# Performance work log

Measured on AMD Instinct MI355X. Metric: run time of the kernel, lower is better.

## Reference

```python
import jax, jax.numpy as jnp
import numpy as np

EMBED = 50
SEQ = 100
NLABEL = 15
HID = 20
VOCAB = 50000
BATCH = 8192


def gru_scan(xs, W, U, b, return_sequences):
    """Keras GRUCell (reset_after=True, gate order z,r,h).
    xs: (B, T, D). W: (D, 3H), U: (H, 3H), b: (2, 3H) [input bias, recurrent bias].
    """
    B = xs.shape[0]
    H = U.shape[0]
    bi, br = b[0], b[1]
    h0 = jnp.zeros((B, H), dtype=xs.dtype)

    def step(h, x_t):
        mx = x_t @ W + bi                      # (B, 3H)
        mh = h @ U + br                        # (B, 3H)
        xz, xr, xh = mx[:, :H], mx[:, H:2*H], mx[:, 2*H:]
        hz, hr, hh_ = mh[:, :H], mh[:, H:2*H], mh[:, 2*H:]
        z = jax.nn.sigmoid(xz + hz)
        r = jax.nn.sigmoid(xr + hr)
        hh = jnp.tanh(xh + r * hh_)
        h_new = z * h + (1.0 - z) * hh
        return h_new, h_new

    xs_t = jnp.swapaxes(xs, 0, 1)              # (T, B, D)
    h_last, hs = jax.lax.scan(step, h0, xs_t)
    if return_sequences:
        return jnp.swapaxes(hs, 0, 1)          # (B, T, H)
    return h_last                               # (B, H)


def setup_inputs() -> dict:
    key = jax.random.key(0)
    ks = jax.random.split(key, 9)
    s = 0.05
    return {
        "x": jax.random.randint(ks[0], (BATCH, SEQ), 0, VOCAB),
        "emb_table": jax.random.normal(ks[1], (VOCAB, EMBED), jnp.float32) * s,
        "W1": jax.random.normal(ks[2], (EMBED, 3 * HID), jnp.float32) * s,
        "U1": jax.random.normal(ks[3], (HID, 3 * HID), jnp.float32) * s,
        "b1": jnp.zeros((2, 3 * HID), jnp.float32),
        "W2": jax.random.normal(ks[4], (HID, 3 * HID), jnp.float32) * s,
        "U2": jax.random.normal(ks[5], (HID, 3 * HID), jnp.float32) * s,
        "b2": jnp.zeros((2, 3 * HID), jnp.float32),
        "Wd": jax.random.normal(ks[6], (HID, NLABEL), jnp.float32) * s,
        "bd": jnp.zeros((NLABEL,), jnp.float32),
        "drop_rate": 0,
    }


def reference(x, emb_table, W1, U1, b1, W2, U2, b2, Wd, bd, drop_rate):
    emb = emb_table[x]                               # (B, T, E)
    seq = gru_scan(emb, W1, U1, b1, return_sequences=True)   # (B, T, H)
    enc = gru_scan(seq, W2, U2, b2, return_sequences=False)  # (B, H)
    # drop_rate == 0 -> tf.nn.dropout is identity
    logits = enc @ Wd + bd                           # (B, 15)
    return logits
```

## Files before the change

### kernel.cpp

```cpp
#include <hip/hip_runtime.h>
#include <hip/hip_bf16.h>
#include <hip/hip_fp16.h>

#define SEQ_T 100
#define HID 20
#define EMB_D 50
#define VOCAB_N 50000
#define TABW 60
#define NTILE 3125
#define BBLK 782

typedef short sh8 __attribute__((ext_vector_type(8)));
typedef float f4  __attribute__((ext_vector_type(4)));

#define OFF_U1P 0
#define OFF_W2P 600
#define OFF_U2P 1200
#define OFF_B1  3600
#define OFF_B2  3720
#define OFF_WD  3840
#define OFF_BD  4140
#define OFF_TAB 4160

__device__ __forceinline__ float ldf(const void* p, int i, int isf) {
  return isf ? ((const float*)p)[i]
             : __bfloat162float(((const __hip_bfloat16*)p)[i]);
}
__device__ __forceinline__ short f2bf(float f) {
  unsigned u = __float_as_uint(f);
  u += 0x7fffu + ((u >> 16) & 1u);
  return (short)(u >> 16);
}
__device__ __forceinline__ float rdl(float v, int l) {
  return __uint_as_float(__builtin_amdgcn_readlane(__float_as_uint(v), l));
}
__device__ __forceinline__ int detect_isf(const void* emb) {
  uint4 dv = ((const uint4*)emb)[threadIdx.x & 63];
  int big = 0;
#pragma unroll
  for (int i = 0; i < 4; ++i) {
    unsigned w = ((const unsigned*)&dv)[i];
    big |= (((w >> 7) & 0xFF) >= 140) | (((w >> 23) & 0xFF) >= 140);
  }
  return (__ballot(big) != 0ull) ? 1 : 0;
}

__global__ __launch_bounds__(256) void build_table(
    const void* __restrict__ emb, const void* __restrict__ W1,
    const void* __restrict__ b1,
    const void* __restrict__ U1, const void* __restrict__ W2,
    const void* __restrict__ U2, const void* __restrict__ b2,
    const void* __restrict__ Wd, const void* __restrict__ bd,
    float* __restrict__ ws)
{
  const int isf = detect_isf(emb);
  if (blockIdx.x == 0) {
    const int t = threadIdx.x;
    unsigned* wsu = (unsigned*)ws;
    for (int i = t; i < 600; i += 256) {
      const int j = i / 10, p = i % 10;
      const int k0 = 2 * p, k1 = 2 * p + 1;
#define PK(M) ((unsigned)__half_as_ushort(__float2half_rn(ldf(M, k0 * 60 + j, isf))) | \
               ((unsigned)__half_as_ushort(__float2half_rn(ldf(M, k1 * 60 + j, isf))) << 16))
      wsu[OFF_U1P + i] = PK(U1);
      wsu[OFF_W2P + i] = PK(W2);
      wsu[OFF_U2P + i] = PK(U2);
#undef PK
    }
    for (int i = t; i < 120; i += 256) {
      ws[OFF_B1 + i] = ldf(b1, i, isf);
      ws[OFF_B2 + i] = ldf(b2, i, isf);
    }
    for (int i = t; i < 300; i += 256) ws[OFF_WD + i] = ldf(Wd, i, isf);
    for (int i = t; i < 15;  i += 256) ws[OFF_BD + i] = ldf(bd, i, isf);
  }

  const int L = threadIdx.x & 63, q = L >> 4, c = L & 15;
  const int wid = blockIdx.x * 4 + (threadIdx.x >> 6);
  float* __restrict__ tab = ws + OFF_TAB;

  __shared__ int4 sB[64][8];
  if (threadIdx.x < 64) {
#pragma unroll
    for (int nt = 0; nt < 4; ++nt) {
      const int col = nt * 16 + c;
      sh8 B0, B1;
#pragma unroll
      for (int jj = 0; jj < 8; ++jj) {
        const int k0 = q * 8 + jj, k1 = 32 + q * 8 + jj;
        B0[jj] = (col < TABW) ? f2bf(ldf(W1, k0 * TABW + col, isf)) : (short)0;
        B1[jj] = (col < TABW && k1 < EMB_D)
                     ? f2bf(ldf(W1, k1 * TABW + col, isf)) : (short)0;
      }
      sB[L][nt * 2]     = *(const int4*)&B0;
      sB[L][nt * 2 + 1] = *(const int4*)&B1;
    }
  }
  float bi[4];
#pragma unroll
  for (int nt = 0; nt < 4; ++nt) {
    const int col = nt * 16 + c;
    bi[nt] = (col < TABW) ? ldf(b1, col, isf) : 0.f;
  }
  __syncthreads();

  for (int tile = wid; tile < NTILE; tile += BBLK * 4) {
    const int v0 = tile * 16;
    sh8 A0, A1;
#pragma unroll
    for (int jj = 0; jj < 8; ++jj) { A0[jj] = 0; A1[jj] = 0; }
    if (!isf) {
      const unsigned short* eb = (const unsigned short*)emb;
      const size_t rb = (size_t)(v0 + c) * EMB_D;
#pragma unroll
      for (int i = 0; i < 4; ++i) {
        unsigned d = *(const unsigned*)(eb + rb + q * 8 + 2 * i);
        A0[2 * i] = (short)(d & 0xffff); A0[2 * i + 1] = (short)(d >> 16);
      }
      const int k1b = 32 + q * 8;
#pragma unroll
      for (int i = 0; i < 4; ++i) {
        const int k = k1b + 2 * i;
        if (k + 1 < EMB_D) {
          unsigned d = *(const unsigned*)(eb + rb + k);
          A1[2 * i] = (short)(d & 0xffff); A1[2 * i + 1] = (short)(d >> 16);
        }
      }
    } else {
      const float* ef = (const float*)emb;
      const size_t rb = (size_t)(v0 + c) * EMB_D;
#pragma unroll
      for (int jj = 0; jj < 8; ++jj) {
        const int k0 = q * 8 + jj, k1 = 32 + q * 8 + jj;
        A0[jj] = f2bf(ef[rb + k0]);
        A1[jj] = (k1 < EMB_D) ? f2bf(ef[rb + k1]) : (short)0;
      }
    }
#pragma unroll
    for (int nt = 0; nt < 4; ++nt) {
      int4 b0i = sB[L][nt * 2], b1i = sB[L][nt * 2 + 1];
      sh8 B0 = *(const sh8*)&b0i, B1 = *(const sh8*)&b1i;
      const int col = nt * 16 + c;
      f4 acc = { bi[nt], bi[nt], bi[nt], bi[nt] };
      acc = __builtin_amdgcn_mfma_f32_16x16x32_bf16(A0, B0, acc, 0, 0, 0);
      acc = __builtin_amdgcn_mfma_f32_16x16x32_bf16(A1, B1, acc, 0, 0, 0);
      if (col < TABW) {
#pragma unroll
        for (int r = 0; r < 4; ++r)
          tab[(size_t)(v0 + q * 4 + r) * TABW + col] = acc[r];
      }
    }
  }
}

__global__ __launch_bounds__(256, 6) void gru_main(
    const int* __restrict__ x, const float* __restrict__ ws,
    const void* __restrict__ emb, void* __restrict__ out)
{
  const int isf = detect_isf(emb);
  const int j = threadIdx.x & 63;
  const int e = __builtin_amdgcn_readfirstlane(blockIdx.x * 4 + (threadIdx.x >> 6));
  const int jc = j < TABW ? j : 0;

  const int* xr = x + (size_t)e * SEQ_T;
  const float* tab = ws + OFF_TAB;
  const int o1 = jc * 40;
  const int jc4 = jc * 4;
  const int a1 = ((j - 20) & 63) * 4;
  const int a2 = ((j + 40) & 63) * 4;
  const float br1 = ws[OFF_B1 + 60 + jc];
  const float bi2 = ws[OFF_B2 + jc];
  const float br2 = ws[OFF_B2 + 60 + jc];

  __shared__ char sbuf[1024];
  const unsigned lb = (unsigned)(uintptr_t)&sbuf[0] + (threadIdx.x >> 6) * 256;
  const int wad = (int)(lb + (j < 20 ? 2 * j : 40 + 2 * (j - 20)));
  const int rad = (int)lb;
  float h2out;

  asm volatile(
    "global_load_dwordx4 v[10:13], %[o1], %[wsp] offset:0\n\t"
    "global_load_dwordx4 v[14:17], %[o1], %[wsp] offset:16\n\t"
    "global_load_dwordx2 v[18:19], %[o1], %[wsp] offset:32\n\t"
    "v_add_u32 v44, 0x960, %[o1]\n\t"
    "v_add_u32 v45, 0x12c0, %[o1]\n\t"
    "global_load_dwordx4 v[20:23], v44, %[wsp] offset:0\n\t"
    "global_load_dwordx4 v[24:27], v44, %[wsp] offset:16\n\t"
    "global_load_dwordx2 v[28:29], v44, %[wsp] offset:32\n\t"
    "global_load_dwordx4 v[30:33], v45, %[wsp] offset:0\n\t"
    "global_load_dwordx4 v[34:37], v45, %[wsp] offset:16\n\t"
    "global_load_dwordx2 v[38:39], v45, %[wsp] offset:32\n\t"
    "v_mov_b32 v40, 0\n\t"
    "v_mov_b32 v41, 0\n\t"
    "v_mov_b32 v66, 0\n\tv_mov_b32 v67, 0\n\t"
    "v_mov_b32 v68, 0\n\tv_mov_b32 v69, 0\n\t"
    "v_mov_b32 v70, 0\n\tv_mov_b32 v71, 0\n\t"
    "v_mov_b32 v72, 0\n\tv_mov_b32 v73, 0\n\t"
    "v_mov_b32 v74, 0\n\tv_mov_b32 v75, 0\n\t"
    "s_load_dword s65, %[xp], 0x0\n\t"
    "s_load_dword s66, %[xp], 0x4\n\t"
    "s_load_dword s68, %[xp], 0x8\n\t"
    "s_waitcnt lgkmcnt(0)\n\t"
    "s_mul_i32 s65, s65, 240\n\t"
    "s_mul_i32 s66, s66, 240\n\t"
    "s_mul_i32 s68, s68, 240\n\t"
    "v_add_u32 v50, s65, %[jc4]\n\t"
    "global_load_dword v52, v50, %[tabp]\n\t"
    "v_add_u32 v50, s66, %[jc4]\n\t"
    "global_load_dword v42, v50, %[tabp]\n\t"
    "v_add_u32 v50, s68, %[jc4]\n\t"
    "global_load_dword v43, v50, %[tabp]\n\t"
    "s_load_dword s65, %[xp], 0xc\n\t"
    "s_load_dword s68, %[xp], 0x10\n\t"
    "s_movk_i32 s64, 0x14\n\t"
    "s_movk_i32 s69, 0x18\n\t"
    "s_movk_i32 s67, 0x32\n\t"
    "s_waitcnt vmcnt(2)\n\t"
    "v_mov_b32 v44, %[br1]\n\t"
    "v_add_f32 v45, v52, v44\n\t"
    "v_mul_f32 v45, 0xbfb8aa3b, v45\n\t"
    "v_exp_f32 v45, v45\n\t"
    "s_nop 1\n\t"
    "v_add_f32 v45, 1.0, v45\n\t"
    "v_rcp_f32 v45, v45\n\t"
    "s_nop 1\n\t"
    "ds_bpermute_b32 v46, %[a1], v45\n\t"
    "s_waitcnt lgkmcnt(0)\n\t"
    "v_fma_f32 v47, v46, v44, v52\n\t"
    "v_mul_f32 v47, 0x4038aa3b, v47\n\t"
    "v_exp_f32 v47, v47\n\t"
    "s_nop 1\n\t"
    "v_add_f32 v47, 1.0, v47\n\t"
    "v_rcp_f32 v47, v47\n\t"
    "s_nop 1\n\t"
    "v_fma_f32 v47, -2.0, v47, 1.0\n\t"
    "ds_bpermute_b32 v46, %[a2], v47\n\t"
    "s_waitcnt lgkmcnt(0)\n\t"
    "v_sub_f32 v48, v40, v46\n\t"
    "v_fma_f32 v40, v45, v48, v46\n\t"
    "v_cvt_f16_f32 v46, v40\n\t"
    "ds_write_b16 %[wad], v46\n\t"
    "ds_read_b128 v[56:59], %[rad]\n\t"
    "ds_read_b128 v[60:63], %[rad] offset:16\n\t"
    "ds_read_b64  v[64:65], %[rad] offset:32\n\t"
    "0:\n\t"
    "s_waitcnt lgkmcnt(0)\n\t"
    "v_dot2_f32_f16 v44, v56, v10, %[br1]\n\t"
    "v_dot2_f32_f16 v51, v56, v20, %[bi2]\n\t"
    "v_dot2_f32_f16 v52, v66, v30, %[br2]\n\t"
    "v_dot2_f32_f16 v44, v57, v11, v44\n\t"
    "v_dot2_f32_f16 v51, v57, v21, v51\n\t"
    "v_dot2_f32_f16 v52, v67, v31, v52\n\t"
    "v_dot2_f32_f16 v44, v58, v12, v44\n\t"
    "v_dot2_f32_f16 v51, v58, v22, v51\n\t"
    "v_dot2_f32_f16 v52, v68, v32, v52\n\t"
    "v_dot2_f32_f16 v44, v59, v13, v44\n\t"
    "v_dot2_f32_f16 v51, v59, v23, v51\n\t"
    "v_dot2_f32_f16 v52, v69, v33, v52\n\t"
    "v_dot2_f32_f16 v44, v60, v14, v44\n\t"
    "v_dot2_f32_f16 v51, v60, v24, v51\n\t"
    "v_dot2_f32_f16 v52, v70, v34, v52\n\t"
    "v_dot2_f32_f16 v44, v61, v15, v44\n\t"
    "v_dot2_f32_f16 v51, v61, v25, v51\n\t"
    "v_dot2_f32_f16 v52, v71, v35, v52\n\t"
    "v_dot2_f32_f16 v44, v62, v16, v44\n\t"
    "v_dot2_f32_f16 v51, v62, v26, v51\n\t"
    "v_dot2_f32_f16 v52, v72, v36, v52\n\t"
    "v_dot2_f32_f16 v44, v63, v17, v44\n\t"
    "v_dot2_f32_f16 v51, v63, v27, v51\n\t"
    "v_dot2_f32_f16 v52, v73, v37, v52\n\t"
    "v_dot2_f32_f16 v44, v64, v18, v44\n\t"
    "v_dot2_f32_f16 v51, v64, v28, v51\n\t"
    "v_dot2_f32_f16 v52, v74, v38, v52\n\t"
    "v_dot2_f32_f16 v44, v65, v19, v44\n\t"
    "v_dot2_f32_f16 v51, v65, v29, v51\n\t"
    "v_dot2_f32_f16 v52, v75, v39, v52\n\t"
    "s_waitcnt vmcnt(1)\n\t"
    "v_add_f32 v45, v42, v44\n\t"
    "v_add_f32 v53, v51, v52\n\t"
    "v_mul_f32 v45, 0xbfb8aa3b, v45\n\t"
    "v_mul_f32 v53, 0xbfb8aa3b, v53\n\t"
    "v_exp_f32 v45, v45\n\t"
    "v_exp_f32 v53, v53\n\t"
    "v_add_f32 v45, 1.0, v45\n\t"
    "v_add_f32 v53, 1.0, v53\n\t"
    "v_rcp_f32 v45, v45\n\t"
    "v_rcp_f32 v53, v53\n\t"
    "ds_bpermute_b32 v46, %[a1], v45\n\t"
    "ds_bpermute_b32 v54, %[a1], v53\n\t"
    "s_mul_i32 s66, s65, 240\n\t"
    "v_add_u32 v50, s66, %[jc4]\n\t"
    "s_waitcnt lgkmcnt(0)\n\t"
    "v_fma_f32 v47, v46, v44, v42\n\t"
    "v_fma_f32 v55, v54, v52, v51\n\t"
    "global_load_dword v42, v50, %[tabp]\n\t"
    "s_min_u32 s64, s64, 396\n\t"
    "s_load_dword s65, %[xp], s64\n\t"
    "s_add_u32 s64, s64, 8\n\t"
    "v_mul_f32 v47, 0x4038aa3b, v47\n\t"
    "v_mul_f32 v55, 0x4038aa3b, v55\n\t"
    "v_exp_f32 v47, v47\n\t"
    "v_exp_f32 v55, v55\n\t"
    "v_add_f32 v47, 1.0, v47\n\t"
    "v_add_f32 v55, 1.0, v55\n\t"
    "v_rcp_f32 v47, v47\n\t"
    "v_rcp_f32 v55, v55\n\t"
    "s_nop 0\n\t"
    "v_fma_f32 v47, -2.0, v47, 1.0\n\t"
    "v_fma_f32 v55, -2.0, v55, 1.0\n\t"
    "ds_bpermute_b32 v46, %[a2], v47\n\t"
    "ds_bpermute_b32 v54, %[a2], v55\n\t"
    "s_waitcnt lgkmcnt(0)\n\t"
    "v_sub_f32 v48, v40, v46\n\t"
    "v_fma_f32 v40, v45, v48, v46\n\t"
    "v_sub_f32 v48, v41, v54\n\t"
    "v_fma_f32 v41, v53, v48, v54\n\t"
    "v_cvt_f16_f32 v46, v40\n\t"
    "v_cvt_f16_f32 v54, v41\n\t"
    "ds_write_b16 %[wad], v46\n\t"
    "ds_write_b16 %[wad], v54 offset:128\n\t"
    "ds_read_b128 v[56:59], %[rad]\n\t"
    "ds_read_b128 v[60:63], %[rad] offset:16\n\t"
    "ds_read_b64  v[64:65], %[rad] offset:32\n\t"
    "ds_read_b128 v[66:69], %[rad] offset:128\n\t"
    "ds_read_b128 v[70:73], %[rad] offset:144\n\t"
    "ds_read_b64  v[74:75], %[rad] offset:160\n\t"
    "s_waitcnt lgkmcnt(0)\n\t"
    "v_dot2_f32_f16 v44, v56, v10, %[br1]\n\t"
    "v_dot2_f32_f16 v51, v56, v20, %[bi2]\n\t"
    "v_dot2_f32_f16 v52, v66, v30, %[br2]\n\t"
    "v_dot2_f32_f16 v44, v57, v11, v44\n\t"
    "v_dot2_f32_f16 v51, v57, v21, v51\n\t"
    "v_dot2_f32_f16 v52, v67, v31, v52\n\t"
    "v_dot2_f32_f16 v44, v58, v12, v44\n\t"
    "v_dot2_f32_f16 v51, v58, v22, v51\n\t"
    "v_dot2_f32_f16 v52, v68, v32, v52\n\t"
    "v_dot2_f32_f16 v44, v59, v13, v44\n\t"
    "v_dot2_f32_f16 v51, v59, v23, v51\n\t"
    "v_dot2_f32_f16 v52, v69, v33, v52\n\t"
    "v_dot2_f32_f16 v44, v60, v14, v44\n\t"
    "v_dot2_f32_f16 v51, v60, v24, v51\n\t"
    "v_dot2_f32_f16 v52, v70, v34, v52\n\t"
    "v_dot2_f32_f16 v44, v61, v15, v44\n\t"
    "v_dot2_f32_f16 v51, v61, v25, v51\n\t"
    "v_dot2_f32_f16 v52, v71, v35, v52\n\t"
    "v_dot2_f32_f16 v44, v62, v16, v44\n\t"
    "v_dot2_f32_f16 v51, v62, v26, v51\n\t"
    "v_dot2_f32_f16 v52, v72, v36, v52\n\t"
    "v_dot2_f32_f16 v44, v63, v17, v44\n\t"
    "v_dot2_f32_f16 v51, v63, v27, v51\n\t"
    "v_dot2_f32_f16 v52, v73, v37, v52\n\t"
    "v_dot2_f32_f16 v44, v64, v18, v44\n\t"
    "v_dot2_f32_f16 v51, v64, v28, v51\n\t"
    "v_dot2_f32_f16 v52, v74, v38, v52\n\t"
    "v_dot2_f32_f16 v44, v65, v19, v44\n\t"
    "v_dot2_f32_f16 v51, v65, v29, v51\n\t"
    "v_dot2_f32_f16 v52, v75, v39, v52\n\t"
    "s_waitcnt vmcnt(1)\n\t"
    "v_add_f32 v45, v43, v44\n\t"
    "v_add_f32 v53, v51, v52\n\t"
    "v_mul_f32 v45, 0xbfb8aa3b, v45\n\t"
    "v_mul_f32 v53, 0xbfb8aa3b, v53\n\t"
    "v_exp_f32 v45, v45\n\t"
    "v_exp_f32 v53, v53\n\t"
    "v_add_f32 v45, 1.0, v45\n\t"
    "v_add_f32 v53, 1.0, v53\n\t"
    "v_rcp_f32 v45, v45\n\t"
    "v_rcp_f32 v53, v53\n\t"
    "ds_bpermute_b32 v46, %[a1], v45\n\t"
    "ds_bpermute_b32 v54, %[a1], v53\n\t"
    "s_mul_i32 s66, s68, 240\n\t"
    "v_add_u32 v50, s66, %[jc4]\n\t"
    "s_waitcnt lgkmcnt(0)\n\t"
    "v_fma_f32 v47, v46, v44, v43\n\t"
    "v_fma_f32 v55, v54, v52, v51\n\t"
    "global_load_dword v43, v50, %[tabp]\n\t"
    "s_min_u32 s69, s69, 392\n\t"
    "s_load_dword s68, %[xp], s69\n\t"
    "s_add_u32 s69, s69, 8\n\t"
    "v_mul_f32 v47, 0x4038aa3b, v47\n\t"
    "v_mul_f32 v55, 0x4038aa3b, v55\n\t"
    "v_exp_f32 v47, v47\n\t"
    "v_exp_f32 v55, v55\n\t"
    "v_add_f32 v47, 1.0, v47\n\t"
    "v_add_f32 v55, 1.0, v55\n\t"
    "v_rcp_f32 v47, v47\n\t"
    "v_rcp_f32 v55, v55\n\t"
    "s_nop 0\n\t"
    "v_fma_f32 v47, -2.0, v47, 1.0\n\t"
    "v_fma_f32 v55, -2.0, v55, 1.0\n\t"
    "ds_bpermute_b32 v46, %[a2], v47\n\t"
    "ds_bpermute_b32 v54, %[a2], v55\n\t"
    "s_waitcnt lgkmcnt(0)\n\t"
    "v_sub_f32 v48, v40, v46\n\t"
    "v_fma_f32 v40, v45, v48, v46\n\t"
    "v_sub_f32 v48, v41, v54\n\t"
    "v_fma_f32 v41, v53, v48, v54\n\t"
    "v_cvt_f16_f32 v46, v40\n\t"
    "v_cvt_f16_f32 v54, v41\n\t"
    "ds_write_b16 %[wad], v46\n\t"
    "ds_write_b16 %[wad], v54 offset:128\n\t"
    "ds_read_b128 v[56:59], %[rad]\n\t"
    "ds_read_b128 v[60:63], %[rad] offset:16\n\t"
    "ds_read_b64  v[64:65], %[rad] offset:32\n\t"
    "ds_read_b128 v[66:69], %[rad] offset:128\n\t"
    "ds_read_b128 v[70:73], %[rad] offset:144\n\t"
    "ds_read_b64  v[74:75], %[rad] offset:160\n\t"
    "s_sub_u32 s67, s67, 1\n\t"
    "s_cmp_lg_u32 s67, 0\n\t"
    "s_cbranch_scc1 0b\n\t"
    "s_waitcnt vmcnt(0) lgkmcnt(0)\n\t"
    "v_mov_b32 %[h2o], v41\n\t"
    : [h2o] "=v"(h2out)
    : [wsp] "s"(ws), [xp] "s"(xr), [tabp] "s"(tab),
      [o1] "v"(o1), [jc4] "v"(jc4), [a1] "v"(a1), [a2] "v"(a2),
      [br1] "v"(br1), [bi2] "v"(bi2), [br2] "v"(br2),
      [wad] "v"(wad), [rad] "v"(rad)
    : "memory", "vcc", "scc",
      "v10","v11","v12","v13","v14","v15","v16","v17","v18","v19",
      "v20","v21","v22","v23","v24","v25","v26","v27","v28","v29",
      "v30","v31","v32","v33","v34","v35","v36","v37","v38","v39",
      "v40","v41","v42","v43","v44","v45","v46","v47","v48","v50",
      "v51","v52","v53","v54","v55",
      "v56","v57","v58","v59","v60","v61","v62","v63","v64","v65",
      "v66","v67","v68","v69","v70","v71","v72","v73","v74","v75",
      "s64","s65","s66","s67","s68","s69");

  if (j < 15) {
    float a = ws[OFF_BD + j];
#pragma unroll
    for (int k = 0; k < HID; ++k)
      a = fmaf(rdl(h2out, k), ws[OFF_WD + k * 15 + j], a);
    if (isf) ((float*)out)[(size_t)e * 15 + j] = a;
    else ((__hip_bfloat16*)out)[(size_t)e * 15 + j] = __float2bfloat16(a);
  }
}

extern "C" void kernel_launch(void* const* d_in, const int* in_sizes, int n_in,
                              void* d_out, int out_size, void* d_ws, size_t ws_size,
                              hipStream_t stream) {
  const int* x    = (const int*)d_in[0];
  const void* emb = d_in[1];
  const void* W1  = d_in[2];
  const void* U1  = d_in[3];
  const void* b1  = d_in[4];
  const void* W2  = d_in[5];
  const void* U2  = d_in[6];
  const void* b2  = d_in[7];
  const void* Wd  = d_in[8];
  const void* bd  = d_in[9];
  float* ws = (float*)d_ws;

  build_table<<<BBLK, 256, 0, stream>>>(
      emb, W1, b1, U1, W2, U2, b2, Wd, bd, ws);
  gru_main<<<2048, 256, 0, stream>>>(x, ws, emb, d_out);
}
```

Baseline: 200.3 us.

## Store token-gate table as fp16 with exp2 scaling folded into weights

Stores the precomputed per-token input-projection table in fp16 instead of fp32, halving the bytes gathered per timestep. The log2e scaling for the sigmoid and tanh exponents is folded into the weights, biases and table entries at build time, so the recurrent loop drops its per-gate multiplies. Launch bounds occupancy hint goes from 6 to 5. This costs fp16 precision loss on the table and gate pre-activations, and adds a conversion instruction per loaded entry.

```diff
diff --git a/kernel.cpp b/kernel.cpp
--- a/kernel.cpp
+++ b/kernel.cpp
@@ -43,6 +43,9 @@
     big |= (((w >> 7) & 0xFF) >= 140) | (((w >> 23) & 0xFF) >= 140);
   }
   return (__ballot(big) != 0ull) ? 1 : 0;
+}
+__device__ __forceinline__ float gsc(int col) {
+  return (col < 40) ? -1.44269504f : 2.88539008f;
 }
 
 __global__ __launch_bounds__(256) void build_table(
@@ -60,16 +63,17 @@
     for (int i = t; i < 600; i += 256) {
       const int j = i / 10, p = i % 10;
       const int k0 = 2 * p, k1 = 2 * p + 1;
-#define PK(M) ((unsigned)__half_as_ushort(__float2half_rn(ldf(M, k0 * 60 + j, isf))) | \
-               ((unsigned)__half_as_ushort(__float2half_rn(ldf(M, k1 * 60 + j, isf))) << 16))
+      const float s = gsc(j);
+#define PK(M) ((unsigned)__half_as_ushort(__float2half_rn(ldf(M, k0 * 60 + j, isf) * s)) | \
+               ((unsigned)__half_as_ushort(__float2half_rn(ldf(M, k1 * 60 + j, isf) * s)) << 16))
       wsu[OFF_U1P + i] = PK(U1);
       wsu[OFF_W2P + i] = PK(W2);
       wsu[OFF_U2P + i] = PK(U2);
 #undef PK
     }
     for (int i = t; i < 120; i += 256) {
-      ws[OFF_B1 + i] = ldf(b1, i, isf);
-      ws[OFF_B2 + i] = ldf(b2, i, isf);
+      ws[OFF_B1 + i] = ldf(b1, i, isf) * (i >= 60 ? gsc(i - 60) : 1.f);
+      ws[OFF_B2 + i] = ldf(b2, i, isf) * gsc(i % 60);
     }
     for (int i = t; i < 300; i += 256) ws[OFF_WD + i] = ldf(Wd, i, isf);
     for (int i = t; i < 15;  i += 256) ws[OFF_BD + i] = ldf(bd, i, isf);
@@ -77,7 +81,7 @@
 
   const int L = threadIdx.x & 63, q = L >> 4, c = L & 15;
   const int wid = blockIdx.x * 4 + (threadIdx.x >> 6);
-  float* __restrict__ tab = ws + OFF_TAB;
+  unsigned short* __restrict__ tab16 = (unsigned short*)(ws + OFF_TAB);
 
   __shared__ int4 sB[64][8];
   if (threadIdx.x < 64) {
@@ -145,15 +149,17 @@
       acc = __builtin_amdgcn_mfma_f32_16x16x32_bf16(A0, B0, acc, 0, 0, 0);
       acc = __builtin_amdgcn_mfma_f32_16x16x32_bf16(A1, B1, acc, 0, 0, 0);
       if (col < TABW) {
+        const float s = gsc(col);
 #pragma unroll
         for (int r = 0; r < 4; ++r)
-          tab[(size_t)(v0 + q * 4 + r) * TABW + col] = acc[r];
+          tab16[(size_t)(v0 + q * 4 + r) * TABW + col] =
+              __half_as_ushort(__float2half_rn(acc[r] * s));
       }
     }
   }
 }
 
-__global__ __launch_bounds__(256, 6) void gru_main(
+__global__ __launch_bounds__(256, 5) void gru_main(
     const int* __restrict__ x, const float* __restrict__ ws,
     const void* __restrict__ emb, void* __restrict__ out)
 {
@@ -163,9 +169,9 @@
   const int jc = j < TABW ? j : 0;
 
   const int* xr = x + (size_t)e * SEQ_T;
-  const float* tab = ws + OFF_TAB;
+  const unsigned short* tab = (const unsigned short*)(ws + OFF_TAB);
   const int o1 = jc * 40;
-  const int jc4 = jc * 4;
+  const int jc2 = jc * 2;
   const int a1 = ((j - 20) & 63) * 4;
   const int a2 = ((j + 40) & 63) * 4;
   const float br1 = ws[OFF_B1 + 60 + jc];
@@ -201,24 +207,24 @@
     "s_load_dword s66, %[xp], 0x4\n\t"
     "s_load_dword s68, %[xp], 0x8\n\t"
     "s_waitcnt lgkmcnt(0)\n\t"
-    "s_mul_i32 s65, s65, 240\n\t"
-    "s_mul_i32 s66, s66, 240\n\t"
-    "s_mul_i32 s68, s68, 240\n\t"
-    "v_add_u32 v50, s65, %[jc4]\n\t"
-    "global_load_dword v52, v50, %[tabp]\n\t"
-    "v_add_u32 v50, s66, %[jc4]\n\t"
-    "global_load_dword v42, v50, %[tabp]\n\t"
-    "v_add_u32 v50, s68, %[jc4]\n\t"
-    "global_load_dword v43, v50, %[tabp]\n\t"
+    "s_mul_i32 s65, s65, 120\n\t"
+    "s_mul_i32 s66, s66, 120\n\t"
+    "s_mul_i32 s68, s68, 120\n\t"
+    "v_add_u32 v50, s65, %[jc2]\n\t"
+    "global_load_ushort v52, v50, %[tabp]\n\t"
+    "v_add_u32 v50, s66, %[jc2]\n\t"
+    "global_load_ushort v42, v50, %[tabp]\n\t"
+    "v_add_u32 v50, s68, %[jc2]\n\t"
+    "global_load_ushort v43, v50, %[tabp]\n\t"
     "s_load_dword s65, %[xp], 0xc\n\t"
     "s_load_dword s68, %[xp], 0x10\n\t"
     "s_movk_i32 s64, 0x14\n\t"
     "s_movk_i32 s69, 0x18\n\t"
     "s_movk_i32 s67, 0x32\n\t"
     "s_waitcnt vmcnt(2)\n\t"
+    "v_cvt_f32_f16 v52, v52\n\t"
     "v_mov_b32 v44, %[br1]\n\t"
     "v_add_f32 v45, v52, v44\n\t"
-    "v_mul_f32 v45, 0xbfb8aa3b, v45\n\t"
     "v_exp_f32 v45, v45\n\t"
     "s_nop 1\n\t"
     "v_add_f32 v45, 1.0, v45\n\t"
@@ -227,7 +233,6 @@
     "ds_bpermute_b32 v46, %[a1], v45\n\t"
     "s_waitcnt lgkmcnt(0)\n\t"
     "v_fma_f32 v47, v46, v44, v52\n\t"
-    "v_mul_f32 v47, 0x4038aa3b, v47\n\t"
     "v_exp_f32 v47, v47\n\t"
     "s_nop 1\n\t"
     "v_add_f32 v47, 1.0, v47\n\t"
@@ -276,10 +281,9 @@
     "v_dot2_f32_f16 v51, v65, v29, v51\n\t"
     "v_dot2_f32_f16 v52, v75, v39, v52\n\t"
     "s_waitcnt vmcnt(1)\n\t"
+    "v_cvt_f32_f16 v42, v42\n\t"
     "v_add_f32 v45, v42, v44\n\t"
     "v_add_f32 v53, v51, v52\n\t"
-    "v_mul_f32 v45, 0xbfb8aa3b, v45\n\t"
-    "v_mul_f32 v53, 0xbfb8aa3b, v53\n\t"
     "v_exp_f32 v45, v45\n\t"
     "v_exp_f32 v53, v53\n\t"
     "v_add_f32 v45, 1.0, v45\n\t"
@@ -288,17 +292,15 @@
     "v_rcp_f32 v53, v53\n\t"
     "ds_bpermute_b32 v46, %[a1], v45\n\t"
     "ds_bpermute_b32 v54, %[a1], v53\n\t"
-    "s_mul_i32 s66, s65, 240\n\t"
-    "v_add_u32 v50, s66, %[jc4]\n\t"
+    "s_mul_i32 s66, s65, 120\n\t"
+    "v_add_u32 v50, s66, %[jc2]\n\t"
     "s_waitcnt lgkmcnt(0)\n\t"
     "v_fma_f32 v47, v46, v44, v42\n\t"
     "v_fma_f32 v55, v54, v52, v51\n\t"
-    "global_load_dword v42, v50, %[tabp]\n\t"
+    "global_load_ushort v42, v50, %[tabp]\n\t"
     "s_min_u32 s64, s64, 396\n\t"
     "s_load_dword s65, %[xp], s64\n\t"
     "s_add_u32 s64, s64, 8\n\t"
-    "v_mul_f32 v47, 0x4038aa3b, v47\n\t"
-    "v_mul_f32 v55, 0x4038aa3b, v55\n\t"
     "v_exp_f32 v47, v47\n\t"
     "v_exp_f32 v55, v55\n\t"
     "v_add_f32 v47, 1.0, v47\n\t"
@@ -357,10 +359,9 @@
     "v_dot2_f32_f16 v51, v65, v29, v51\n\t"
     "v_dot2_f32_f16 v52, v75, v39, v52\n\t"
     "s_waitcnt vmcnt(1)\n\t"
+    "v_cvt_f32_f16 v43, v43\n\t"
     "v_add_f32 v45, v43, v44\n\t"
     "v_add_f32 v53, v51, v52\n\t"
-    "v_mul_f32 v45, 0xbfb8aa3b, v45\n\t"
-    "v_mul_f32 v53, 0xbfb8aa3b, v53\n\t"
     "v_exp_f32 v45, v45\n\t"
     "v_exp_f32 v53, v53\n\t"
     "v_add_f32 v45, 1.0, v45\n\t"
@@ -369,17 +370,15 @@
     "v_rcp_f32 v53, v53\n\t"
     "ds_bpermute_b32 v46, %[a1], v45\n\t"
     "ds_bpermute_b32 v54, %[a1], v53\n\t"
-    "s_mul_i32 s66, s68, 240\n\t"
-    "v_add_u32 v50, s66, %[jc4]\n\t"
+    "s_mul_i32 s66, s68, 120\n\t"
+    "v_add_u32 v50, s66, %[jc2]\n\t"
     "s_waitcnt lgkmcnt(0)\n\t"
     "v_fma_f32 v47, v46, v44, v43\n\t"
     "v_fma_f32 v55, v54, v52, v51\n\t"
-    "global_load_dword v43, v50, %[tabp]\n\t"
+    "global_load_ushort v43, v50, %[tabp]\n\t"
     "s_min_u32 s69, s69, 392\n\t"
     "s_load_dword s68, %[xp], s69\n\t"
     "s_add_u32 s69, s69, 8\n\t"
-    "v_mul_f32 v47, 0x4038aa3b, v47\n\t"
-    "v_mul_f32 v55, 0x4038aa3b, v55\n\t"
     "v_exp_f32 v47, v47\n\t"
     "v_exp_f32 v55, v55\n\t"
     "v_add_f32 v47, 1.0, v47\n\t"
@@ -413,7 +412,7 @@
     "v_mov_b32 %[h2o], v41\n\t"
     : [h2o] "=v"(h2out)
     : [wsp] "s"(ws), [xp] "s"(xr), [tabp] "s"(tab),
-      [o1] "v"(o1), [jc4] "v"(jc4), [a1] "v"(a1), [a2] "v"(a2),
+      [o1] "v"(o1), [jc2] "v"(jc2), [a1] "v"(a1), [a2] "v"(a2),
       [br1] "v"(br1), [bi2] "v"(bi2), [br2] "v"(br2),
       [wad] "v"(wad), [rad] "v"(rad)
     : "memory", "vcc", "scc",
```

New measurement: 197.7 us. No clear change (-1.3%).
